# Kernel optimization log

Measured on AMD Instinct MI355X. Metric: run time of the kernel, lower is better.

## Reference

```python
import jax, jax.numpy as jnp
import numpy as np

N = 50000
E = 800000
HID = 128
OUT = 64
HEADS = 4
NEG_SLOPE = 0.2


def gat_layer(x, edge_index, W, att_src, att_dst, bias):
    """PyG-style GATConv: shared linear for src/dst, additive attention,
    self-loops, segment softmax over incoming edges, concat heads + bias."""
    n = x.shape[0]
    H, C = att_src.shape
    # add self loops (PyG default add_self_loops=True)
    loops = jnp.arange(n, dtype=edge_index.dtype)
    src = jnp.concatenate([edge_index[0], loops])  # message sources j
    dst = jnp.concatenate([edge_index[1], loops])  # aggregation targets i
    xl = (x @ W).reshape(n, H, C)                  # [N,H,C]
    a_s = jnp.einsum('nhc,hc->nh', xl, att_src)    # [N,H]
    a_d = jnp.einsum('nhc,hc->nh', xl, att_dst)    # [N,H]
    e = jax.nn.leaky_relu(a_s[src] + a_d[dst], NEG_SLOPE)   # [E',H]
    m = jax.ops.segment_max(e, dst, num_segments=n)         # stable softmax
    e = jnp.exp(e - m[dst])
    denom = jax.ops.segment_sum(e, dst, num_segments=n)
    alpha = e / (denom[dst] + 1e-16)                        # [E',H]
    msg = xl[src] * alpha[:, :, None]                       # [E',H,C]
    out = jax.ops.segment_sum(msg, dst, num_segments=n)     # [N,H,C]
    return out.reshape(n, H * C) + bias


def setup_inputs() -> dict:
    key = jax.random.key(0)
    ks = jax.random.split(key, 16)
    C = HID // HEADS  # per-head channels = 32
    x = jax.random.normal(ks[0], (N, HID), dtype=jnp.float32)
    edge_indices = jax.random.randint(ks[1], (3, 2, E), 0, N, dtype=jnp.int32)
    s = 0.1
    inp = {
        'x': x,
        'edge_indices': edge_indices,
        'W1': jax.random.normal(ks[2], (HID, HEADS * C), dtype=jnp.float32) * s,
        'as1': jax.random.normal(ks[3], (HEADS, C), dtype=jnp.float32) * s,
        'ad1': jax.random.normal(ks[4], (HEADS, C), dtype=jnp.float32) * s,
        'b1': jnp.zeros((HEADS * C,), dtype=jnp.float32),
        'W2': jax.random.normal(ks[5], (HID, HEADS * C), dtype=jnp.float32) * s,
        'as2': jax.random.normal(ks[6], (HEADS, C), dtype=jnp.float32) * s,
        'ad2': jax.random.normal(ks[7], (HEADS, C), dtype=jnp.float32) * s,
        'b2': jnp.zeros((HEADS * C,), dtype=jnp.float32),
        'W3': jax.random.normal(ks[8], (HID, OUT), dtype=jnp.float32) * s,
        'as3': jax.random.normal(ks[9], (1, OUT), dtype=jnp.float32) * s,
        'ad3': jax.random.normal(ks[10], (1, OUT), dtype=jnp.float32) * s,
        'b3': jnp.zeros((OUT,), dtype=jnp.float32),
    }
    return inp


def reference(x, edge_indices, W1, as1, ad1, b1, W2, as2, ad2, b2, W3, as3, ad3, b3):
    h = jax.nn.relu(gat_layer(x, edge_indices[0], W1, as1, ad1, b1))
    h = jax.nn.relu(gat_layer(h, edge_indices[1], W2, as2, ad2, b2))
    out = gat_layer(h, edge_indices[2], W3, as3, ad3, b3)  # no ReLU on last layer
    return out
```

## Files before the change

kernel.cpp:

```cpp
#include <hip/hip_runtime.h>

typedef unsigned short u16;
typedef unsigned int u32;
typedef __attribute__((ext_vector_type(8))) short short8;
typedef __attribute__((ext_vector_type(4))) float f32x4;

#define HID 128

static inline int cdiv(long long a, int b) { return (int)((a + b - 1) / b); }

__device__ __forceinline__ float bfbits(u32 u) { union { u32 u; float f; } c; c.u = u; return c.f; }
__device__ __forceinline__ u16 f2bf(float f) {
  union { float f; u32 u; } c; c.f = f;
  u32 u = c.u;
  return (u16)((u + 0x7fffu + ((u >> 16) & 1u)) >> 16);
}
__device__ __forceinline__ u32 pack2bf(float a, float b) {
  return (u32)f2bf(a) | ((u32)f2bf(b) << 16);
}

template <int COUT, int HEADS, bool BF16IN>
__global__ __launch_bounds__(256) void gemm_attn_mfma(
    const void* __restrict__ HinV, const u16* __restrict__ WT,
    const float* __restrict__ attS, const float* __restrict__ attD,
    u16* __restrict__ XL, float* __restrict__ aS, float* __restrict__ aD, int n) {
  constexpr int NT = COUT / 16;
  constexpr int C = COUT / HEADS;
  constexpr int TPH = C / 16;

  int t = threadIdx.x;
  int wv = t >> 6, ln = t & 63;
  int lrow = ln & 15;
  int lk = ln >> 4;
  int row = blockIdx.x * 64 + wv * 16 + lrow;
  bool ok = (row < n);
  int rowc = ok ? row : (n - 1);

  short8 bb[4];
  if (BF16IN) {
    const u16* hp = (const u16*)HinV + (size_t)rowc * HID;
#pragma unroll
    for (int kb = 0; kb < 4; ++kb)
      bb[kb] = *(const short8*)(hp + kb * 32 + lk * 8);
  } else {
    const float* hp = (const float*)HinV + (size_t)rowc * HID;
    float4 hv[8];
#pragma unroll
    for (int kb = 0; kb < 4; ++kb) {
      hv[2 * kb] = *(const float4*)(hp + kb * 32 + lk * 8);
      hv[2 * kb + 1] = *(const float4*)(hp + kb * 32 + lk * 8 + 4);
    }
#pragma unroll
    for (int kb = 0; kb < 4; ++kb) {
      union { short8 s; u32 u[4]; } pk;
      float4 h0 = hv[2 * kb], h1 = hv[2 * kb + 1];
      pk.u[0] = pack2bf(h0.x, h0.y);
      pk.u[1] = pack2bf(h0.z, h0.w);
      pk.u[2] = pack2bf(h1.x, h1.y);
      pk.u[3] = pack2bf(h1.z, h1.w);
      bb[kb] = pk.s;
    }
  }

  f32x4 acc[NT];
#pragma unroll
  for (int ct = 0; ct < NT; ++ct) acc[ct] = {0.f, 0.f, 0.f, 0.f};

#pragma unroll
  for (int kb = 0; kb < 4; ++kb) {
    const u16* wp = WT + (size_t)lrow * HID + kb * 32 + lk * 8;
#pragma unroll
    for (int ct = 0; ct < NT; ++ct) {
      short8 aw = *(const short8*)(wp + (size_t)ct * 16 * HID);
      acc[ct] = __builtin_amdgcn_mfma_f32_16x16x32_bf16(aw, bb[kb], acc[ct], 0, 0, 0);
    }
  }

  float pS[HEADS], pD[HEADS];
#pragma unroll
  for (int h = 0; h < HEADS; ++h) { pS[h] = 0.f; pD[h] = 0.f; }
#pragma unroll
  for (int ct = 0; ct < NT; ++ct) {
    float4 sv = *(const float4*)(attS + ct * 16 + lk * 4);
    float4 dv = *(const float4*)(attD + ct * 16 + lk * 4);
    int h = ct / TPH;
    pS[h] += acc[ct][0] * sv.x + acc[ct][1] * sv.y + acc[ct][2] * sv.z + acc[ct][3] * sv.w;
    pD[h] += acc[ct][0] * dv.x + acc[ct][1] * dv.y + acc[ct][2] * dv.z + acc[ct][3] * dv.w;
  }
#pragma unroll
  for (int h = 0; h < HEADS; ++h) {
    pS[h] += __shfl_xor(pS[h], 16);
    pS[h] += __shfl_xor(pS[h], 32);
    pD[h] += __shfl_xor(pD[h], 16);
    pD[h] += __shfl_xor(pD[h], 32);
  }
  if (lk == 0 && ok) {
    if (HEADS == 4) {
      *(float4*)(aS + (size_t)row * 4) = make_float4(pS[0], pS[1], pS[2], pS[3]);
      *(float4*)(aD + (size_t)row * 4) = make_float4(pD[0], pD[1], pD[2], pD[3]);
    } else {
      aS[row] = pS[0];
      aD[row] = pD[0];
    }
  }

  if (ok) {
    u32* Xp = (u32*)XL + (size_t)row * (COUT / 2);
#pragma unroll
    for (int ct = 0; ct < NT; ++ct) {
      *(uint2*)(Xp + ct * 8 + lk * 2) =
          make_uint2(pack2bf(acc[ct][0], acc[ct][1]), pack2bf(acc[ct][2], acc[ct][3]));
    }
  }
}

#define PSTR 16

__global__ __launch_bounds__(256) void bucket_hist_prep(
    const int* __restrict__ ei, int* __restrict__ cntP, int e4, int rem, int E, int NB,
    const float* __restrict__ W1, const float* __restrict__ W2,
    const float* __restrict__ W3, u16* __restrict__ wt1, u16* __restrict__ wt2,
    u16* __restrict__ wt3) {
  if (blockIdx.y == 3) {
    int bx = blockIdx.x;
    if (bx >= 160) return;
    int y = (bx >= 128) ? 2 : (bx >= 64 ? 1 : 0);
    int b0 = (y == 0) ? 0 : ((y == 1) ? 64 : 128);
    const float* W = (y == 0) ? W1 : ((y == 1) ? W2 : W3);
    u16* WT = (y == 0) ? wt1 : ((y == 1) ? wt2 : wt3);
    int cout = (y == 2) ? 64 : 128;
    int idx = (bx - b0) * 256 + threadIdx.x;
    if (idx < 128 * cout) {
      int k = idx / cout, c = idx - k * cout;
      WT[c * 128 + k] = f2bf(W[idx]);
    }
    return;
  }
  int L = blockIdx.y;
  const int* dst = ei + (size_t)(2 * L + 1) * E;
  __shared__ int cnt[256];
  int t = threadIdx.x;
  cnt[t] = 0;
  __syncthreads();
  int gbase = blockIdx.x * 1024 + t;
#pragma unroll
  for (int u = 0; u < 4; ++u) {
    int g = gbase + u * 256;
    if (g < e4) {
      int4 d = *(const int4*)(dst + g * 4);
      atomicAdd(&cnt[d.x >> 8], 1);
      atomicAdd(&cnt[d.y >> 8], 1);
      atomicAdd(&cnt[d.z >> 8], 1);
      atomicAdd(&cnt[d.w >> 8], 1);
    }
  }
  if (blockIdx.x == 0 && t < rem) atomicAdd(&cnt[dst[e4 * 4 + t] >> 8], 1);
  __syncthreads();
  int c = cnt[t];
  if (t < NB && c > 0) atomicAdd(&cntP[(L * NB + t) * PSTR], c);
}

__global__ __launch_bounds__(256) void bucket_scan(const int* __restrict__ cntP,
                                                   int* __restrict__ bucketOff,
                                                   int* __restrict__ curP, int NB, int E) {
  int L = blockIdx.x;
  int t = threadIdx.x;
  int lane = t & 63, wid = t >> 6;
  __shared__ int wpart[4];
  int v = (t < NB) ? cntP[(L * NB + t) * PSTR] : 0;
  int inc = v;
#pragma unroll
  for (int off = 1; off < 64; off <<= 1) {
    int w = __shfl_up(inc, (unsigned)off, 64);
    if (lane >= off) inc += w;
  }
  if (lane == 63) wpart[wid] = inc;
  __syncthreads();
  if (t == 0) {
    int a = 0;
#pragma unroll
    for (int k = 0; k < 4; ++k) { int tmp = wpart[k]; wpart[k] = a; a += tmp; }
  }
  __syncthreads();
  int ex = wpart[wid] + inc - v;
  if (t < NB) {
    bucketOff[L * (NB + 1) + t] = ex;
    curP[(L * NB + t) * PSTR] = ex;
  }
  if (t == 0) bucketOff[L * (NB + 1) + NB] = E;
}

__global__ __launch_bounds__(256) void bucket_scatter(const int* __restrict__ ei,
                                                      int* __restrict__ curP,
                                                      int2* __restrict__ pairsAll,
                                                      int e4, int rem, int E, int NB) {
  int L = blockIdx.y;
  const int* src = ei + (size_t)(2 * L) * E;
  const int* dst = src + E;
  int2* pairs = pairsAll + (size_t)L * E;
  __shared__ int cnt[256];
  __shared__ int baseS[256];
  int t = threadIdx.x;
  cnt[t] = 0;
  __syncthreads();

  int gbase = blockIdx.x * 1024 + t;
  int4 dv[4], sv[4];
  bool val[4];
#pragma unroll
  for (int u = 0; u < 4; ++u) {
    int g = gbase + u * 256;
    val[u] = (g < e4);
    if (val[u]) {
      dv[u] = *(const int4*)(dst + g * 4);
      sv[u] = *(const int4*)(src + g * 4);
      atomicAdd(&cnt[dv[u].x >> 8], 1);
      atomicAdd(&cnt[dv[u].y >> 8], 1);
      atomicAdd(&cnt[dv[u].z >> 8], 1);
      atomicAdd(&cnt[dv[u].w >> 8], 1);
    }
  }
  int tailS = 0, tailD = 0;
  bool hasTail = (blockIdx.x == 0 && t < rem);
  if (hasTail) {
    tailD = dst[e4 * 4 + t];
    tailS = src[e4 * 4 + t];
    atomicAdd(&cnt[tailD >> 8], 1);
  }
  __syncthreads();
  int c = cnt[t];
  if (t < NB && c > 0) baseS[t] = atomicAdd(&curP[(L * NB + t) * PSTR], c);
  __syncthreads();
  cnt[t] = 0;
  __syncthreads();
#pragma unroll
  for (int u = 0; u < 4; ++u) {
    if (val[u]) {
      int b, p;
      b = dv[u].x >> 8; p = atomicAdd(&cnt[b], 1); pairs[baseS[b] + p] = make_int2(sv[u].x, dv[u].x);
      b = dv[u].y >> 8; p = atomicAdd(&cnt[b], 1); pairs[baseS[b] + p] = make_int2(sv[u].y, dv[u].y);
      b = dv[u].z >> 8; p = atomicAdd(&cnt[b], 1); pairs[baseS[b] + p] = make_int2(sv[u].z, dv[u].z);
      b = dv[u].w >> 8; p = atomicAdd(&cnt[b], 1); pairs[baseS[b] + p] = make_int2(sv[u].w, dv[u].w);
    }
  }
  if (hasTail) {
    int b = tailD >> 8;
    int p = atomicAdd(&cnt[b], 1);
    pairs[baseS[b] + p] = make_int2(tailS, tailD);
  }
}

__global__ __launch_bounds__(256) void csr_finalize(const int2* __restrict__ pairsAll,
                                                    const int* __restrict__ bucketOff,
                                                    int* __restrict__ indptrAll,
                                                    int* __restrict__ srcIdxAll,
                                                    int N, int E, int NB) {
  int L = blockIdx.y, b = blockIdx.x;
  const int2* pairs = pairsAll + (size_t)L * E;
  int* indptr = indptrAll + (size_t)L * (N + 1);
  int* srcL = srcIdxAll + (size_t)L * (E + N);
  int base = b << 8;
  int nodes = min(256, N - base);
  int p0 = bucketOff[L * (NB + 1) + b];
  int p1 = bucketOff[L * (NB + 1) + b + 1];

  __shared__ int cnt[256];
  __shared__ int wpart[4];
  int t = threadIdx.x;
  int lane = t & 63, wid = t >> 6;
  cnt[t] = 0;
  __syncthreads();

  for (int i = p0 + t; i < p1; i += 256) atomicAdd(&cnt[pairs[i].y - base], 1);
  __syncthreads();

  int v = (t < nodes) ? cnt[t] + 1 : 0;
  int inc = v;
#pragma unroll
  for (int off = 1; off < 64; off <<= 1) {
    int w = __shfl_up(inc, (unsigned)off, 64);
    if (lane >= off) inc += w;
  }
  if (lane == 63) wpart[wid] = inc;
  __syncthreads();
  if (t == 0) {
    int a = 0;
#pragma unroll
    for (int k = 0; k < 4; ++k) { int tmp = wpart[k]; wpart[k] = a; a += tmp; }
  }
  __syncthreads();
  int ex = wpart[wid] + inc - v;
  __syncthreads();
  if (t < nodes) {
    int segStart = p0 + base + ex;
    indptr[base + t] = segStart;
    srcL[segStart] = base + t;
    cnt[t] = segStart + 1;
  }
  if (b == NB - 1 && t == 0) indptr[N] = E + N;
  __syncthreads();

  for (int i = p0 + t; i < p1; i += 256) {
    int2 pr = pairs[i];
    int p = atomicAdd(&cnt[pr.y - base], 1);
    srcL[p] = pr.x;
  }
}

template <int COUT, int HEADS, bool RELU, bool OUTBF>
__global__ __launch_bounds__(256) void aggregate(
    const u16* __restrict__ XL, const float* __restrict__ aS, const float* __restrict__ aD,
    const int* __restrict__ indptr, const int* __restrict__ srcIdx,
    const float* __restrict__ bias, void* __restrict__ outV, int n) {
  constexpr int LPN = COUT / 8;
  constexpr int NPW = 64 / LPN;
  constexpr int C = COUT / HEADS;

  int wid = (blockIdx.x * blockDim.x + threadIdx.x) >> 6;
  int lane = threadIdx.x & 63;
  int sub = lane / LPN;
  int cl = lane % LPN;
  int i = wid * NPW + sub;
  bool ok = (i < n);
  int ic = ok ? i : (n - 1);

  int col0 = cl * 8;
  int h = col0 / C;
  float ad = aD[(size_t)ic * HEADS + h];
  int e0 = indptr[ic], e1 = indptr[ic + 1];
  int deg = e1 - e0;

  const u32* XL32 = (const u32*)XL;
  float s = 0.f;
  float acc[8];
#pragma unroll
  for (int v = 0; v < 8; ++v) acc[v] = 0.f;

  int jn = srcIdx[e0];
  float an = aS[(size_t)jn * HEADS + h];
  uint4 qn = *(const uint4*)(XL32 + (size_t)jn * (COUT / 2) + cl * 4);

#pragma unroll 2
  for (int k = 0; k < deg; ++k) {
    float ac = an;
    uint4 qc = qn;
    if (k + 1 < deg) {
      int j2 = srcIdx[e0 + k + 1];
      an = aS[(size_t)j2 * HEADS + h];
      qn = *(const uint4*)(XL32 + (size_t)j2 * (COUT / 2) + cl * 4);
    }
    float l = ac + ad;
    l = (l >= 0.f) ? l : 0.2f * l;
    float el = __expf(fminf(l, 60.f));
    s += el;
    acc[0] += el * bfbits(qc.x << 16);
    acc[1] += el * bfbits(qc.x & 0xffff0000u);
    acc[2] += el * bfbits(qc.y << 16);
    acc[3] += el * bfbits(qc.y & 0xffff0000u);
    acc[4] += el * bfbits(qc.z << 16);
    acc[5] += el * bfbits(qc.z & 0xffff0000u);
    acc[6] += el * bfbits(qc.w << 16);
    acc[7] += el * bfbits(qc.w & 0xffff0000u);
  }

  if (!ok) return;
  float inv = 1.f / (s + 1e-16f);
  float o[8];
#pragma unroll
  for (int v = 0; v < 8; ++v) {
    o[v] = acc[v] * inv + bias[col0 + v];
    if (RELU) o[v] = fmaxf(o[v], 0.f);
  }
  if (OUTBF) {
    u32* op = (u32*)outV + (size_t)i * (COUT / 2) + cl * 4;
    *(uint4*)op = make_uint4(pack2bf(o[0], o[1]), pack2bf(o[2], o[3]),
                             pack2bf(o[4], o[5]), pack2bf(o[6], o[7]));
  } else {
    float* op = (float*)outV + (size_t)i * COUT + col0;
    *(float4*)op = make_float4(o[0], o[1], o[2], o[3]);
    *(float4*)(op + 4) = make_float4(o[4], o[5], o[6], o[7]);
  }
}

extern "C" void kernel_launch(void* const* d_in, const int* in_sizes, int n_in,
                              void* d_out, int out_size, void* d_ws, size_t ws_size,
                              hipStream_t stream) {
  const float* x = (const float*)d_in[0];
  const int* ei = (const int*)d_in[1];
  const float* W1 = (const float*)d_in[2];
  const float* as1 = (const float*)d_in[3];
  const float* ad1 = (const float*)d_in[4];
  const float* b1 = (const float*)d_in[5];
  const float* W2 = (const float*)d_in[6];
  const float* as2 = (const float*)d_in[7];
  const float* ad2 = (const float*)d_in[8];
  const float* b2 = (const float*)d_in[9];
  const float* W3 = (const float*)d_in[10];
  const float* as3 = (const float*)d_in[11];
  const float* ad3 = (const float*)d_in[12];
  const float* b3 = (const float*)d_in[13];

  int N = in_sizes[0] / HID;
  int E = in_sizes[1] / 6;
  int NB = cdiv(N, 256);

  char* w = (char*)d_ws;
  auto alloc = [&](size_t bytes) {
    void* q = (void*)w;
    w += (bytes + 255) & ~(size_t)255;
    return q;
  };
  u16* bufH = (u16*)alloc((size_t)N * HID * 2);
  u16* bufXL = (u16*)alloc((size_t)N * HID * 2);
  float* aS = (float*)alloc((size_t)N * 4 * 4);
  float* aD = (float*)alloc((size_t)N * 4 * 4);
  u16* wt1 = (u16*)alloc((size_t)128 * 128 * 2);
  u16* wt2 = (u16*)alloc((size_t)128 * 128 * 2);
  u16* wt3 = (u16*)alloc((size_t)64 * 128 * 2);
  int* cntP = (int*)alloc((size_t)3 * NB * PSTR * 4);
  int* curP = (int*)alloc((size_t)3 * NB * PSTR * 4);
  int* bucketOff = (int*)alloc((size_t)3 * (NB + 1) * 4);
  int2* pairsAll = (int2*)alloc((size_t)3 * E * 8);
  int* indptrAll = (int*)alloc((size_t)3 * (N + 1) * 4);
  int* srcIdxAll = (int*)alloc((size_t)3 * (E + N) * 4);

  int e4 = E >> 2, rem = E & 3;
  int gx = cdiv(e4, 1024);
  int gxh = (gx > 160) ? gx : 160;

  hipMemsetAsync(cntP, 0, (size_t)3 * NB * PSTR * 4, stream);
  {
    dim3 g(gxh, 4);
    bucket_hist_prep<<<g, 256, 0, stream>>>(ei, cntP, e4, rem, E, NB,
                                            W1, W2, W3, wt1, wt2, wt3);
  }
  bucket_scan<<<3, 256, 0, stream>>>(cntP, bucketOff, curP, NB, E);
  {
    dim3 g(gx, 3);
    bucket_scatter<<<g, 256, 0, stream>>>(ei, curP, pairsAll, e4, rem, E, NB);
  }
  {
    dim3 g(NB, 3);
    csr_finalize<<<g, 256, 0, stream>>>(pairsAll, bucketOff, indptrAll, srcIdxAll, N, E, NB);
  }

  gemm_attn_mfma<128, 4, false><<<cdiv(N, 64), 256, 0, stream>>>(
      x, wt1, as1, ad1, bufXL, aS, aD, N);
  aggregate<128, 4, true, true><<<cdiv(N, 16), 256, 0, stream>>>(
      bufXL, aS, aD, indptrAll, srcIdxAll, b1, bufH, N);
  gemm_attn_mfma<128, 4, true><<<cdiv(N, 64), 256, 0, stream>>>(
      bufH, wt2, as2, ad2, bufXL, aS, aD, N);
  aggregate<128, 4, true, true><<<cdiv(N, 16), 256, 0, stream>>>(
      bufXL, aS, aD, indptrAll + (N + 1), srcIdxAll + (size_t)(E + N), b2, bufH, N);
  gemm_attn_mfma<64, 1, true><<<cdiv(N, 64), 256, 0, stream>>>(
      bufH, wt3, as3, ad3, bufXL, aS, aD, N);
  aggregate<64, 1, false, false><<<cdiv(N, 32), 256, 0, stream>>>(
      bufXL, aS, aD, indptrAll + 2 * (N + 1), srcIdxAll + (size_t)2 * (E + N), b3,
      d_out, N);
}
```

Baseline: 330.1 us.

## Fuse layer-1 GEMM into scatter, pack edge pairs, deepen aggregate prefetch

Runs the first-layer GEMM/attention as extra blocks (blockIdx.y==3) of the bucket scatter kernel, so the GEMM overlaps the CSR build and one launch is removed. Packs each (src, dst-within-bucket) pair into a single 32-bit word instead of an int2, halving the pair buffer traffic in scatter and finalize. This packing assumes node ids fit in 24 bits. The aggregate loop now keeps four gathers in flight instead of one, using a software pipeline of depth 4, and gains an occupancy hint in launch_bounds. The cost is higher register pressure in aggregate, plus a scatter kernel whose blocks do uneven amounts of work.

```diff
diff --git a/kernel.cpp b/kernel.cpp
--- a/kernel.cpp
+++ b/kernel.cpp
@@ -20,19 +20,18 @@
 }
 
 template <int COUT, int HEADS, bool BF16IN>
-__global__ __launch_bounds__(256) void gemm_attn_mfma(
-    const void* __restrict__ HinV, const u16* __restrict__ WT,
+__device__ __forceinline__ void gemm_body(
+    int bx, int t, const void* __restrict__ HinV, const u16* __restrict__ WT,
     const float* __restrict__ attS, const float* __restrict__ attD,
     u16* __restrict__ XL, float* __restrict__ aS, float* __restrict__ aD, int n) {
   constexpr int NT = COUT / 16;
   constexpr int C = COUT / HEADS;
   constexpr int TPH = C / 16;
 
-  int t = threadIdx.x;
   int wv = t >> 6, ln = t & 63;
   int lrow = ln & 15;
   int lk = ln >> 4;
-  int row = blockIdx.x * 64 + wv * 16 + lrow;
+  int row = bx * 64 + wv * 16 + lrow;
   bool ok = (row < n);
   int rowc = ok ? row : (n - 1);
 
@@ -112,6 +111,15 @@
           make_uint2(pack2bf(acc[ct][0], acc[ct][1]), pack2bf(acc[ct][2], acc[ct][3]));
     }
   }
+}
+
+template <int COUT, int HEADS, bool BF16IN>
+__global__ __launch_bounds__(256) void gemm_attn_mfma(
+    const void* __restrict__ HinV, const u16* __restrict__ WT,
+    const float* __restrict__ attS, const float* __restrict__ attD,
+    u16* __restrict__ XL, float* __restrict__ aS, float* __restrict__ aD, int n) {
+  gemm_body<COUT, HEADS, BF16IN>(blockIdx.x, threadIdx.x, HinV, WT, attS, attD,
+                                 XL, aS, aD, n);
 }
 
 #define PSTR 16
@@ -190,14 +198,22 @@
   if (t == 0) bucketOff[L * (NB + 1) + NB] = E;
 }
 
-__global__ __launch_bounds__(256) void bucket_scatter(const int* __restrict__ ei,
-                                                      int* __restrict__ curP,
-                                                      int2* __restrict__ pairsAll,
-                                                      int e4, int rem, int E, int NB) {
+__global__ __launch_bounds__(256) void bucket_scatter_gemm(
+    const int* __restrict__ ei, int* __restrict__ curP, u32* __restrict__ pairsAll,
+    int e4, int rem, int E, int NB,
+    const float* __restrict__ x, const u16* __restrict__ wt1,
+    const float* __restrict__ as1, const float* __restrict__ ad1,
+    u16* __restrict__ XL, float* __restrict__ aS, float* __restrict__ aD,
+    int n, int ngb) {
+  if (blockIdx.y == 3) {
+    if ((int)blockIdx.x < ngb)
+      gemm_body<128, 4, false>(blockIdx.x, threadIdx.x, x, wt1, as1, ad1, XL, aS, aD, n);
+    return;
+  }
   int L = blockIdx.y;
   const int* src = ei + (size_t)(2 * L) * E;
   const int* dst = src + E;
-  int2* pairs = pairsAll + (size_t)L * E;
+  u32* pairs = pairsAll + (size_t)L * E;
   __shared__ int cnt[256];
   __shared__ int baseS[256];
   int t = threadIdx.x;
@@ -237,26 +253,30 @@
   for (int u = 0; u < 4; ++u) {
     if (val[u]) {
       int b, p;
-      b = dv[u].x >> 8; p = atomicAdd(&cnt[b], 1); pairs[baseS[b] + p] = make_int2(sv[u].x, dv[u].x);
-      b = dv[u].y >> 8; p = atomicAdd(&cnt[b], 1); pairs[baseS[b] + p] = make_int2(sv[u].y, dv[u].y);
-      b = dv[u].z >> 8; p = atomicAdd(&cnt[b], 1); pairs[baseS[b] + p] = make_int2(sv[u].z, dv[u].z);
-      b = dv[u].w >> 8; p = atomicAdd(&cnt[b], 1); pairs[baseS[b] + p] = make_int2(sv[u].w, dv[u].w);
+      b = dv[u].x >> 8; p = atomicAdd(&cnt[b], 1);
+      pairs[baseS[b] + p] = ((u32)(dv[u].x & 0xff) << 24) | (u32)sv[u].x;
+      b = dv[u].y >> 8; p = atomicAdd(&cnt[b], 1);
+      pairs[baseS[b] + p] = ((u32)(dv[u].y & 0xff) << 24) | (u32)sv[u].y;
+      b = dv[u].z >> 8; p = atomicAdd(&cnt[b], 1);
+      pairs[baseS[b] + p] = ((u32)(dv[u].z & 0xff) << 24) | (u32)sv[u].z;
+      b = dv[u].w >> 8; p = atomicAdd(&cnt[b], 1);
+      pairs[baseS[b] + p] = ((u32)(dv[u].w & 0xff) << 24) | (u32)sv[u].w;
     }
   }
   if (hasTail) {
     int b = tailD >> 8;
     int p = atomicAdd(&cnt[b], 1);
-    pairs[baseS[b] + p] = make_int2(tailS, tailD);
-  }
-}
-
-__global__ __launch_bounds__(256) void csr_finalize(const int2* __restrict__ pairsAll,
+    pairs[baseS[b] + p] = ((u32)(tailD & 0xff) << 24) | (u32)tailS;
+  }
+}
+
+__global__ __launch_bounds__(256) void csr_finalize(const u32* __restrict__ pairsAll,
                                                     const int* __restrict__ bucketOff,
                                                     int* __restrict__ indptrAll,
                                                     int* __restrict__ srcIdxAll,
                                                     int N, int E, int NB) {
   int L = blockIdx.y, b = blockIdx.x;
-  const int2* pairs = pairsAll + (size_t)L * E;
+  const u32* pairs = pairsAll + (size_t)L * E;
   int* indptr = indptrAll + (size_t)L * (N + 1);
   int* srcL = srcIdxAll + (size_t)L * (E + N);
   int base = b << 8;
@@ -271,7 +291,7 @@
   cnt[t] = 0;
   __syncthreads();
 
-  for (int i = p0 + t; i < p1; i += 256) atomicAdd(&cnt[pairs[i].y - base], 1);
+  for (int i = p0 + t; i < p1; i += 256) atomicAdd(&cnt[pairs[i] >> 24], 1);
   __syncthreads();
 
   int v = (t < nodes) ? cnt[t] + 1 : 0;
@@ -301,20 +321,21 @@
   __syncthreads();
 
   for (int i = p0 + t; i < p1; i += 256) {
-    int2 pr = pairs[i];
-    int p = atomicAdd(&cnt[pr.y - base], 1);
-    srcL[p] = pr.x;
+    u32 pk = pairs[i];
+    int p = atomicAdd(&cnt[pk >> 24], 1);
+    srcL[p] = (int)(pk & 0xffffffu);
   }
 }
 
 template <int COUT, int HEADS, bool RELU, bool OUTBF>
-__global__ __launch_bounds__(256) void aggregate(
+__global__ __launch_bounds__(256, 8) void aggregate(
     const u16* __restrict__ XL, const float* __restrict__ aS, const float* __restrict__ aD,
     const int* __restrict__ indptr, const int* __restrict__ srcIdx,
     const float* __restrict__ bias, void* __restrict__ outV, int n) {
   constexpr int LPN = COUT / 8;
   constexpr int NPW = 64 / LPN;
   constexpr int C = COUT / HEADS;
+  constexpr int D = 4;
 
   int wid = (blockIdx.x * blockDim.x + threadIdx.x) >> 6;
   int lane = threadIdx.x & 63;
@@ -327,8 +348,8 @@
   int col0 = cl * 8;
   int h = col0 / C;
   float ad = aD[(size_t)ic * HEADS + h];
-  int e0 = indptr[ic], e1 = indptr[ic + 1];
-  int deg = e1 - e0;
+  int e0 = indptr[ic];
+  int deg = indptr[ic + 1] - e0;
 
   const u32* XL32 = (const u32*)XL;
   float s = 0.f;
@@ -336,31 +357,42 @@
 #pragma unroll
   for (int v = 0; v < 8; ++v) acc[v] = 0.f;
 
-  int jn = srcIdx[e0];
-  float an = aS[(size_t)jn * HEADS + h];
-  uint4 qn = *(const uint4*)(XL32 + (size_t)jn * (COUT / 2) + cl * 4);
-
-#pragma unroll 2
-  for (int k = 0; k < deg; ++k) {
-    float ac = an;
-    uint4 qc = qn;
-    if (k + 1 < deg) {
-      int j2 = srcIdx[e0 + k + 1];
-      an = aS[(size_t)j2 * HEADS + h];
-      qn = *(const uint4*)(XL32 + (size_t)j2 * (COUT / 2) + cl * 4);
-    }
-    float l = ac + ad;
+  auto fetch = [&](int k, float& av, uint4& q) {
+    int kk = (k < deg) ? k : 0;
+    int j = srcIdx[e0 + kk];
+    av = aS[(size_t)j * HEADS + h];
+    q = *(const uint4*)(XL32 + (size_t)j * (COUT / 2) + cl * 4);
+  };
+  auto consume = [&](int k, float av, const uint4& q) {
+    if (k >= deg) return;
+    float l = av + ad;
     l = (l >= 0.f) ? l : 0.2f * l;
     float el = __expf(fminf(l, 60.f));
     s += el;
-    acc[0] += el * bfbits(qc.x << 16);
-    acc[1] += el * bfbits(qc.x & 0xffff0000u);
-    acc[2] += el * bfbits(qc.y << 16);
-    acc[3] += el * bfbits(qc.y & 0xffff0000u);
-    acc[4] += el * bfbits(qc.z << 16);
-    acc[5] += el * bfbits(qc.z & 0xffff0000u);
-    acc[6] += el * bfbits(qc.w << 16);
-    acc[7] += el * bfbits(qc.w & 0xffff0000u);
+    acc[0] += el * bfbits(q.x << 16);
+    acc[1] += el * bfbits(q.x & 0xffff0000u);
+    acc[2] += el * bfbits(q.y << 16);
+    acc[3] += el * bfbits(q.y & 0xffff0000u);
+    acc[4] += el * bfbits(q.z << 16);
+    acc[5] += el * bfbits(q.z & 0xffff0000u);
+    acc[6] += el * bfbits(q.w << 16);
+    acc[7] += el * bfbits(q.w & 0xffff0000u);
+  };
+
+  float aP[D];
+  uint4 qP[D];
+#pragma unroll
+  for (int j = 0; j < D; ++j) fetch(j, aP[j], qP[j]);
+
+  for (int k0 = 0; k0 < deg; k0 += D) {
+    bool more = (k0 + D < deg);
+#pragma unroll
+    for (int j = 0; j < D; ++j) {
+      float av = aP[j];
+      uint4 q = qP[j];
+      if (more) fetch(k0 + D + j, aP[j], qP[j]);
+      consume(k0 + j, av, q);
+    }
   }
 
   if (!ok) return;
@@ -420,13 +452,15 @@
   int* cntP = (int*)alloc((size_t)3 * NB * PSTR * 4);
   int* curP = (int*)alloc((size_t)3 * NB * PSTR * 4);
   int* bucketOff = (int*)alloc((size_t)3 * (NB + 1) * 4);
-  int2* pairsAll = (int2*)alloc((size_t)3 * E * 8);
+  u32* pairsAll = (u32*)alloc((size_t)3 * E * 4);
   int* indptrAll = (int*)alloc((size_t)3 * (N + 1) * 4);
   int* srcIdxAll = (int*)alloc((size_t)3 * (E + N) * 4);
 
   int e4 = E >> 2, rem = E & 3;
   int gx = cdiv(e4, 1024);
+  int ngb = cdiv(N, 64);
   int gxh = (gx > 160) ? gx : 160;
+  int gxs = (gx > ngb) ? gx : ngb;
 
   hipMemsetAsync(cntP, 0, (size_t)3 * NB * PSTR * 4, stream);
   {
@@ -436,16 +470,15 @@
   }
   bucket_scan<<<3, 256, 0, stream>>>(cntP, bucketOff, curP, NB, E);
   {
-    dim3 g(gx, 3);
-    bucket_scatter<<<g, 256, 0, stream>>>(ei, curP, pairsAll, e4, rem, E, NB);
+    dim3 g(gxs, 4);
+    bucket_scatter_gemm<<<g, 256, 0, stream>>>(ei, curP, pairsAll, e4, rem, E, NB,
+                                               x, wt1, as1, ad1, bufXL, aS, aD, N, ngb);
   }
   {
     dim3 g(NB, 3);
     csr_finalize<<<g, 256, 0, stream>>>(pairsAll, bucketOff, indptrAll, srcIdxAll, N, E, NB);
   }
 
-  gemm_attn_mfma<128, 4, false><<<cdiv(N, 64), 256, 0, stream>>>(
-      x, wt1, as1, ad1, bufXL, aS, aD, N);
   aggregate<128, 4, true, true><<<cdiv(N, 16), 256, 0, stream>>>(
       bufXL, aS, aD, indptrAll, srcIdxAll, b1, bufH, N);
   gemm_attn_mfma<128, 4, true><<<cdiv(N, 64), 256, 0, stream>>>(
```

New measurement: 323.5 us. 1.02x faster.
